# Optimization experiments

Measured on AMD Instinct MI355X. Metric: run time of the kernel, lower is better.

Reference implementation:

```python
import jax, jax.numpy as jnp
import numpy as np

B, S, D = 2, 2048, 2048
H, G, HD = 16, 8, 128          # query heads, kv groups, head_dim
GS = H // G                     # group size (queries per kv head)
EPS = 1e-6


def _rmsnorm(x, scale):
    # Qwen3-compatible: upcast to f32, rms over last dim, scale
    xf = x.astype(jnp.float32)
    ms = jnp.mean(xf * xf, axis=-1, keepdims=True)
    return (xf * jax.lax.rsqrt(ms + EPS) * scale).astype(x.dtype)


def _rope(x, cos, sin):
    # x: (b, h, s, hd); cos/sin: (s, hd) rotate-half convention
    hd = x.shape[-1]
    x1, x2 = x[..., : hd // 2], x[..., hd // 2 :]
    rotated = jnp.concatenate([-x2, x1], axis=-1)
    s = x.shape[2]
    c = cos[None, None, :s, :]
    sn = sin[None, None, :s, :]
    return (x * c + rotated * sn).astype(x.dtype)


def setup_inputs() -> dict:
    key = jax.random.key(0)
    ks = jax.random.split(key, 8)
    x = jax.random.normal(ks[0], (B, S, D), jnp.float32)
    # causal mask: True = masked (future positions)
    mask = jnp.triu(jnp.ones((S, S), dtype=bool), k=1)
    # RoPE tables, rotate-half convention (cat(angles, angles))
    inv_freq = 1.0 / (10000.0 ** (np.arange(0, HD, 2, dtype=np.float32) / HD))
    angles = np.arange(S, dtype=np.float32)[:, None] * inv_freq[None, :]
    angles = np.concatenate([angles, angles], axis=-1)  # (S, HD)
    cos = jnp.asarray(np.cos(angles))
    sin = jnp.asarray(np.sin(angles))
    std = 0.02
    Wq = jax.random.normal(ks[1], (D, H * HD), jnp.float32) * std
    Wk = jax.random.normal(ks[2], (D, G * HD), jnp.float32) * std
    Wv = jax.random.normal(ks[3], (D, G * HD), jnp.float32) * std
    Wo = jax.random.normal(ks[4], (H * HD, D), jnp.float32) * std
    q_scale = jnp.ones((HD,), jnp.float32)
    k_scale = jnp.ones((HD,), jnp.float32)
    return {"x": x, "mask": mask, "cos": cos, "sin": sin,
            "Wq": Wq, "Wk": Wk, "Wv": Wv, "Wo": Wo,
            "q_scale": q_scale, "k_scale": k_scale}


def reference(x, mask, cos, sin, Wq, Wk, Wv, Wo, q_scale, k_scale):
    b, s, _ = x.shape
    q = (x @ Wq).reshape(b, s, H, HD).transpose(0, 2, 1, 3)   # (b,H,s,hd)
    k = (x @ Wk).reshape(b, s, G, HD).transpose(0, 2, 1, 3)   # (b,G,s,hd)
    v = (x @ Wv).reshape(b, s, G, HD).transpose(0, 2, 1, 3)   # (b,G,s,hd)
    q = _rmsnorm(q, q_scale)
    k = _rmsnorm(k, k_scale)
    q = _rope(q, cos, sin)
    k = _rope(k, cos, sin)
    # grouped attention: avoid repeat_interleave by grouping query heads
    qg = q.reshape(b, G, GS, s, HD)
    scores = jnp.einsum('bghqd,bgkd->bghqk', qg, k)           # (b,G,GS,s,s)
    scores = jnp.where(mask[None, None, None, :, :], -jnp.inf, scores)
    weights = jax.nn.softmax(scores / jnp.sqrt(jnp.float32(HD)), axis=-1)
    ctx = jnp.einsum('bghqk,bgkd->bghqd', weights, v)          # (b,G,GS,s,hd)
    ctx = ctx.reshape(b, H, s, HD).transpose(0, 2, 1, 3).reshape(b, s, H * HD)
    return ctx @ Wo
```

## Files before the change

kernel.cpp:

```cpp
#include <hip/hip_runtime.h>
#include <stdint.h>

#define S_LEN 2048
#define NH 16
#define NG 8
#define HDIM 128

typedef __bf16 bf16x8 __attribute__((ext_vector_type(8)));
typedef float f32x4 __attribute__((ext_vector_type(4)));

#define MFMA16(a, b, c) __builtin_amdgcn_mfma_f32_16x16x32_bf16((a), (b), (c), 0, 0, 0)

__device__ __forceinline__ uint16_t f2bf(float f) {
  union { float f; uint32_t u; } v; v.f = f;
  return (uint16_t)((v.u + 0x7fffu + ((v.u >> 16) & 1u)) >> 16);
}

__device__ __forceinline__ void gload16(const void* g, void* l) {
  __builtin_amdgcn_global_load_lds(
      (__attribute__((address_space(1))) const void*)g,
      (__attribute__((address_space(3))) void*)l, 16, 0, 0);
}

__global__ __launch_bounds__(256) void cvt_x_kernel(
    const float* __restrict__ x, uint16_t* __restrict__ xb, int n4) {
  int i = blockIdx.x * 256 + threadIdx.x;
  if (i >= n4) return;
  float4 v = ((const float4*)x)[i];
  ushort4 o;
  o.x = f2bf(v.x); o.y = f2bf(v.y); o.z = f2bf(v.z); o.w = f2bf(v.w);
  ((ushort4*)xb)[i] = o;
}

__global__ __launch_bounds__(256) void trans_cvt_kernel(
    const float* __restrict__ src, uint16_t* __restrict__ dst, int K, int N) {
  __shared__ float T[32][33];
  int n0 = blockIdx.x * 32, k0 = blockIdx.y * 32;
  int tx = threadIdx.x & 31, ty = threadIdx.x >> 5;
  #pragma unroll
  for (int i = 0; i < 4; ++i)
    T[ty + i * 8][tx] = src[(size_t)(k0 + ty + i * 8) * N + n0 + tx];
  __syncthreads();
  #pragma unroll
  for (int i = 0; i < 4; ++i)
    dst[(size_t)(n0 + ty + i * 8) * K + k0 + tx] = f2bf(T[tx][ty + i * 8]);
}

__global__ __launch_bounds__(256) void gemm_bt_kernel(
    const uint16_t* __restrict__ A, const uint16_t* __restrict__ BT,
    float* __restrict__ C, int M, int N, int K) {
  __shared__ uint8_t smem[32768];
  uint16_t* As = (uint16_t*)smem;
  uint16_t* Bs = (uint16_t*)(smem + 16384);
  const int tid = threadIdx.x, lane = tid & 63, wid = tid >> 6;
  const int l15 = lane & 15, l4 = lane >> 4;
  const int m0 = blockIdx.y * 128, n0 = blockIdx.x * 128;
  const int wm = (wid >> 1) * 64, wn = (wid & 1) * 64;
  const int s_row = lane >> 3, s_col = (lane & 7) * 8;

  f32x4 acc[4][4];
  #pragma unroll
  for (int i = 0; i < 4; ++i)
    #pragma unroll
    for (int j = 0; j < 4; ++j) acc[i][j] = (f32x4){0.f, 0.f, 0.f, 0.f};

  for (int k0 = 0; k0 < K; k0 += 64) {
    #pragma unroll
    for (int i = 0; i < 4; ++i) {
      int chunk = wid * 4 + i;
      int row = chunk * 8 + s_row;
      gload16(A + (size_t)(m0 + row) * K + k0 + s_col, As + chunk * 512);
    }
    #pragma unroll
    for (int i = 0; i < 4; ++i) {
      int chunk = wid * 4 + i;
      int row = chunk * 8 + s_row;
      gload16(BT + (size_t)(n0 + row) * K + k0 + s_col, Bs + chunk * 512);
    }
    __syncthreads();
    #pragma unroll
    for (int kk = 0; kk < 2; ++kk) {
      bf16x8 af[4], bfr[4];
      #pragma unroll
      for (int mi = 0; mi < 4; ++mi)
        af[mi] = *(const bf16x8*)(As + (wm + mi * 16 + l15) * 64 + kk * 32 + l4 * 8);
      #pragma unroll
      for (int ni = 0; ni < 4; ++ni)
        bfr[ni] = *(const bf16x8*)(Bs + (wn + ni * 16 + l15) * 64 + kk * 32 + l4 * 8);
      #pragma unroll
      for (int mi = 0; mi < 4; ++mi)
        #pragma unroll
        for (int ni = 0; ni < 4; ++ni)
          acc[mi][ni] = MFMA16(af[mi], bfr[ni], acc[mi][ni]);
    }
    __syncthreads();
  }
  #pragma unroll
  for (int mi = 0; mi < 4; ++mi)
    #pragma unroll
    for (int ni = 0; ni < 4; ++ni) {
      float* dst = C + (size_t)(m0 + wm + mi * 16 + l4 * 4) * N + n0 + wn + ni * 16 + l15;
      #pragma unroll
      for (int r = 0; r < 4; ++r) dst[(size_t)r * N] = acc[mi][ni][r];
    }
}

__global__ __launch_bounds__(256) void qk_rope_kernel(
    const float* __restrict__ QKV, const float* __restrict__ cosb,
    const float* __restrict__ sinb, const float* __restrict__ qs,
    const float* __restrict__ ks, uint16_t* __restrict__ Qb,
    uint16_t* __restrict__ Kb) {
  const int task = blockIdx.x * 4 + (threadIdx.x >> 6);
  const int lane = threadIdx.x & 63;
  const int hh = task % 24;
  const int row = task / 24;
  const int s = row & (S_LEN - 1);
  const int b = row >> 11;
  const float c1 = cosb[s * 128 + lane], c2 = cosb[s * 128 + 64 + lane];
  const float s1 = sinb[s * 128 + lane], s2 = sinb[s * 128 + 64 + lane];
  const float* src = QKV + (size_t)row * 4096;
  float v1, v2, sc1, sc2, outscale;
  uint16_t* dst;
  if (hh < 16) {
    v1 = src[hh * 128 + lane]; v2 = src[hh * 128 + 64 + lane];
    sc1 = qs[lane]; sc2 = qs[lane + 64];
    outscale = 0.088388347648318447f;
    dst = Qb + ((size_t)(b * NH + hh) * S_LEN + s) * 128;
  } else {
    int g = hh - 16;
    v1 = src[2048 + g * 128 + lane]; v2 = src[2048 + g * 128 + 64 + lane];
    sc1 = ks[lane]; sc2 = ks[lane + 64];
    outscale = 1.0f;
    dst = Kb + ((size_t)(b * NG + g) * S_LEN + s) * 128;
  }
  float ss = v1 * v1 + v2 * v2;
  #pragma unroll
  for (int o = 1; o < 64; o <<= 1) ss += __shfl_xor(ss, o);
  float inv = rsqrtf(ss * (1.0f / 128.0f) + 1e-6f);
  float n1 = v1 * inv * sc1, n2 = v2 * inv * sc2;
  dst[lane] = f2bf((n1 * c1 - n2 * s1) * outscale);
  dst[lane + 64] = f2bf((n2 * c2 + n1 * s2) * outscale);
}

__global__ __launch_bounds__(256) void v_trans_kernel(
    const float* __restrict__ QKV, uint16_t* __restrict__ Vt) {
  __shared__ uint16_t T[128][72];
  const int s0 = blockIdx.x * 64;
  const int bg = blockIdx.y;
  const int b = bg >> 3, g = bg & 7;
  const int tid = threadIdx.x;
  const int tc = tid & 127, tr = tid >> 7;
  const float* src = QKV + ((size_t)(b * S_LEN + s0)) * 4096 + 3072 + g * 128;
  #pragma unroll
  for (int i = 0; i < 32; ++i) {
    int r = i * 2 + tr;
    T[tc][r] = f2bf(src[(size_t)r * 4096 + tc]);
  }
  __syncthreads();
  uint16_t* dst = Vt + (size_t)bg * 128 * S_LEN + s0;
  #pragma unroll
  for (int i = 0; i < 32; ++i) {
    int idx = i * 256 + tid;
    int d = idx >> 6, sof = idx & 63;
    dst[(size_t)d * S_LEN + sof] = T[d][sof];
  }
}

__global__ __launch_bounds__(256) void attn_kernel(
    const uint16_t* __restrict__ Qb, const uint16_t* __restrict__ Kb,
    const uint16_t* __restrict__ Vt, uint16_t* __restrict__ Ctx) {
  __shared__ uint8_t smem[65536 + 4 * 2304];
  const int tid = threadIdx.x, lane = tid & 63, wid = tid >> 6;
  uint16_t* Ps = (uint16_t*)(smem + 65536) + wid * 1152;
  const int l15 = lane & 15, l4 = lane >> 4;

  const int bh = blockIdx.y;
  const int b = bh >> 4, h = bh & 15;
  const int bg = b * NG + (h >> 1);

  const uint16_t* Qh = Qb + (size_t)bh * S_LEN * HDIM;
  const uint16_t* Kh = Kb + (size_t)bg * S_LEN * HDIM;
  const uint16_t* Vh = Vt + (size_t)bg * HDIM * S_LEN;

  const int k_row = lane >> 4, k_c = lane & 15;
  const int v_row = lane >> 3, v_c = lane & 7;

#define STAGE(kt_, buf_)                                                      \
  do {                                                                        \
    const int kv0_ = (kt_) * 64;                                              \
    uint16_t* KsB_ = (uint16_t*)(smem + (buf_) * 16384);                      \
    uint16_t* VsB_ = (uint16_t*)(smem + 32768 + (buf_) * 16384);              \
    _Pragma("unroll")                                                         \
    for (int i_ = 0; i_ < 4; ++i_) {                                          \
      int chunk_ = wid * 4 + i_;                                              \
      int row_ = chunk_ * 4 + k_row;                                          \
      int sc_ = (k_c ^ (row_ & 7)) * 8;                                       \
      gload16(Kh + (size_t)(kv0_ + row_) * HDIM + sc_, KsB_ + chunk_ * 512);  \
    }                                                                         \
    _Pragma("unroll")                                                         \
    for (int i_ = 0; i_ < 4; ++i_) {                                          \
      int chunk_ = wid * 4 + i_;                                              \
      int row_ = chunk_ * 8 + v_row;                                          \
      int sc_ = (v_c ^ (row_ & 7)) * 8;                                       \
      gload16(Vh + (size_t)row_ * S_LEN + kv0_ + sc_, VsB_ + chunk_ * 512);   \
    }                                                                         \
  } while (0)

  for (int half = 0; half < 2; ++half) {
    const int qtile = half ? (31 - (int)blockIdx.x) : (int)blockIdx.x;
    const int q0 = qtile * 64;
    const int qrow = q0 + wid * 16 + l15;

    bf16x8 qf[4];
    #pragma unroll
    for (int kk = 0; kk < 4; ++kk)
      qf[kk] = *(const bf16x8*)(Qh + (size_t)qrow * HDIM + kk * 32 + l4 * 8);

    f32x4 acc[8];
    #pragma unroll
    for (int i = 0; i < 8; ++i) acc[i] = (f32x4){0.f, 0.f, 0.f, 0.f};
    float mrun = -1e30f, lrun = 0.f;

    const int nt = qtile + 1;
    int cur = 0;
    STAGE(0, 0);
    asm volatile("s_waitcnt vmcnt(0)\ns_barrier" ::: "memory");

    for (int kt = 0; kt < nt; ++kt) {
      const int kv0 = kt * 64;
      if (kt + 1 < nt) STAGE(kt + 1, cur ^ 1);

      uint16_t* Ks = (uint16_t*)(smem + cur * 16384);
      uint16_t* Vs = (uint16_t*)(smem + 32768 + cur * 16384);

      f32x4 sc[4];
      #pragma unroll
      for (int i = 0; i < 4; ++i) sc[i] = (f32x4){0.f, 0.f, 0.f, 0.f};
      __builtin_amdgcn_s_setprio(1);
      #pragma unroll
      for (int kk = 0; kk < 4; ++kk) {
        #pragma unroll
        for (int kc = 0; kc < 4; ++kc) {
          int key = kc * 16 + l15;
          int cc = (kk * 4 + l4) ^ (key & 7);
          bf16x8 kf = *(const bf16x8*)(Ks + key * 128 + cc * 8);
          sc[kc] = MFMA16(kf, qf[kk], sc[kc]);
        }
      }
      __builtin_amdgcn_s_setprio(0);
      if (kt == nt - 1) {
        #pragma unroll
        for (int kc = 0; kc < 4; ++kc)
          #pragma unroll
          for (int r = 0; r < 4; ++r)
            if (kv0 + kc * 16 + l4 * 4 + r > qrow) sc[kc][r] = -1e30f;
      }
      float tmax = -1e30f;
      #pragma unroll
      for (int kc = 0; kc < 4; ++kc)
        #pragma unroll
        for (int r = 0; r < 4; ++r) tmax = fmaxf(tmax, sc[kc][r]);
      tmax = fmaxf(tmax, __shfl_xor(tmax, 16));
      tmax = fmaxf(tmax, __shfl_xor(tmax, 32));
      float mnew = fmaxf(mrun, tmax);
      float corr = __expf(mrun - mnew);
      float tsum = 0.f;
      #pragma unroll
      for (int kc = 0; kc < 4; ++kc) {
        float p0 = __expf(sc[kc][0] - mnew);
        float p1 = __expf(sc[kc][1] - mnew);
        float p2 = __expf(sc[kc][2] - mnew);
        float p3 = __expf(sc[kc][3] - mnew);
        tsum += (p0 + p1) + (p2 + p3);
        ushort4 pw;
        pw.x = f2bf(p0); pw.y = f2bf(p1); pw.z = f2bf(p2); pw.w = f2bf(p3);
        *(ushort4*)(Ps + l15 * 72 + kc * 16 + l4 * 4) = pw;
      }
      tsum += __shfl_xor(tsum, 16);
      tsum += __shfl_xor(tsum, 32);
      lrun = lrun * corr + tsum;
      mrun = mnew;
      #pragma unroll
      for (int d0 = 0; d0 < 8; ++d0) acc[d0] *= corr;

      __builtin_amdgcn_s_setprio(1);
      #pragma unroll
      for (int hf = 0; hf < 2; ++hf) {
        bf16x8 pf = *(const bf16x8*)(Ps + l15 * 72 + hf * 32 + l4 * 8);
        #pragma unroll
        for (int d0 = 0; d0 < 8; ++d0) {
          int d = d0 * 16 + l15;
          int cc = (hf * 4 + l4) ^ (d & 7);
          bf16x8 vf = *(const bf16x8*)(Vs + d * 64 + cc * 8);
          acc[d0] = MFMA16(vf, pf, acc[d0]);
        }
      }
      __builtin_amdgcn_s_setprio(0);

      asm volatile("s_waitcnt vmcnt(0)\ns_barrier" ::: "memory");
      cur ^= 1;
    }

    float inv = 1.0f / lrun;
    uint16_t* dst = Ctx + ((size_t)(b * S_LEN + qrow) * NH + h) * HDIM;
    #pragma unroll
    for (int d0 = 0; d0 < 8; ++d0) {
      ushort4 o;
      o.x = f2bf(acc[d0][0] * inv);
      o.y = f2bf(acc[d0][1] * inv);
      o.z = f2bf(acc[d0][2] * inv);
      o.w = f2bf(acc[d0][3] * inv);
      *(ushort4*)(dst + d0 * 16 + l4 * 4) = o;
    }
  }
#undef STAGE
}

extern "C" void kernel_launch(void* const* d_in, const int* in_sizes, int n_in,
                              void* d_out, int out_size, void* d_ws, size_t ws_size,
                              hipStream_t stream) {
  const float* x    = (const float*)d_in[0];
  const float* cosb = (const float*)d_in[2];
  const float* sinb = (const float*)d_in[3];
  const float* Wq   = (const float*)d_in[4];
  const float* Wk   = (const float*)d_in[5];
  const float* Wv   = (const float*)d_in[6];
  const float* Wo   = (const float*)d_in[7];
  const float* qs   = (const float*)d_in[8];
  const float* ks   = (const float*)d_in[9];

  char* ws = (char*)d_ws;
  uint16_t* Xb    = (uint16_t*)(ws);
  uint16_t* WallT = (uint16_t*)(ws + (16ull << 20));
  uint16_t* WoT   = (uint16_t*)(ws + (32ull << 20));
  float*    QKV   = (float*)   (ws + (40ull << 20));
  uint16_t* Qb    = (uint16_t*)(ws + (104ull << 20));
  uint16_t* Kb    = (uint16_t*)(ws + (120ull << 20));
  uint16_t* Vt    = (uint16_t*)(ws + (128ull << 20));
  uint16_t* Ctx   = (uint16_t*)(ws + (136ull << 20));
  float* out = (float*)d_out;

  cvt_x_kernel<<<8192, 256, 0, stream>>>(x, Xb, 2097152);
  trans_cvt_kernel<<<dim3(64, 64), 256, 0, stream>>>(Wq, WallT, 2048, 2048);
  trans_cvt_kernel<<<dim3(32, 64), 256, 0, stream>>>(Wk, WallT + 2048 * 2048, 2048, 1024);
  trans_cvt_kernel<<<dim3(32, 64), 256, 0, stream>>>(Wv, WallT + 3072 * 2048, 2048, 1024);
  trans_cvt_kernel<<<dim3(64, 64), 256, 0, stream>>>(Wo, WoT, 2048, 2048);
  gemm_bt_kernel<<<dim3(32, 32), 256, 0, stream>>>(Xb, WallT, QKV, 4096, 4096, 2048);
  qk_rope_kernel<<<24576, 256, 0, stream>>>(QKV, cosb, sinb, qs, ks, Qb, Kb);
  v_trans_kernel<<<dim3(32, 16), 256, 0, stream>>>(QKV, Vt);
  attn_kernel<<<dim3(16, 32), 256, 0, stream>>>(Qb, Kb, Vt, Ctx);
  gemm_bt_kernel<<<dim3(16, 32), 256, 0, stream>>>(Ctx, WoT, out, 4096, 2048, 2048);
}
```

Baseline: 392.3 us.

## Replace GEMM with 8-wave double-buffered pipelined kernel with swizzled LDS

Replaces the simple 128x128 single-buffered GEMM with a 512-thread kernel using 256x256 (QKV) or 128x256 (output) tiles. The K loop is split into 32-wide halves, double-buffered in dynamic LDS with XOR-swizzled layout, and global-to-LDS loads are interleaved with MFMA phases using barriers, waitcnt control and s_setprio. It also remaps block IDs for XCD-aware L2 locality. The aim is to hide load latency and avoid LDS bank conflicts, at the cost of large LDS use and a complex barrier schedule that lowers occupancy.

New measurement: 358.3 us. 8.7% less time.

```diff
diff --git a/kernel.cpp b/kernel.cpp
--- a/kernel.cpp
+++ b/kernel.cpp
@@ -46,63 +46,144 @@
     dst[(size_t)(n0 + ty + i * 8) * K + k0 + tx] = f2bf(T[tx][ty + i * 8]);
 }
 
-__global__ __launch_bounds__(256) void gemm_bt_kernel(
+template <int NISSUE>
+__device__ __forceinline__ void stage_half(const uint16_t* __restrict__ g,
+                                           int ldg, char* lds, int tid) {
+  #pragma unroll
+  for (int i = 0; i < NISSUE; ++i) {
+    int ch = i * 512 + tid;
+    int pair = ch >> 3, slotd = ch & 7;
+    int slotl = slotd ^ (pair & 7);
+    int row = pair * 2 + (slotl >> 2), c2 = slotl & 3;
+    gload16(g + (size_t)row * ldg + c2 * 8, lds + ch * 16);
+  }
+}
+
+__device__ __forceinline__ bf16x8 ldsfrag(const char* half_base, int row, int l4) {
+  int pair = row >> 1;
+  int slot = ((row & 1) << 2) | l4;
+  return *(const bf16x8*)(half_base + pair * 128 + ((slot ^ (pair & 7)) * 16));
+}
+
+#define BAR() asm volatile("s_barrier" ::: "memory")
+
+template <int BM>
+__global__ __launch_bounds__(512, 2) void gemm8p_kernel(
     const uint16_t* __restrict__ A, const uint16_t* __restrict__ BT,
-    float* __restrict__ C, int M, int N, int K) {
-  __shared__ uint8_t smem[32768];
-  uint16_t* As = (uint16_t*)smem;
-  uint16_t* Bs = (uint16_t*)(smem + 16384);
-  const int tid = threadIdx.x, lane = tid & 63, wid = tid >> 6;
+    float* __restrict__ C, int M, int N, int K, int gridN) {
+  extern __shared__ char smem[];
+  constexpr int MI = BM / 32;
+  constexpr int LA = BM / 128;
+  constexpr int ABYTES = BM * 64;
+  const int tid = threadIdx.x, lane = tid & 63;
+  const int wid = tid >> 6;
   const int l15 = lane & 15, l4 = lane >> 4;
-  const int m0 = blockIdx.y * 128, n0 = blockIdx.x * 128;
-  const int wm = (wid >> 1) * 64, wn = (wid & 1) * 64;
-  const int s_row = lane >> 3, s_col = (lane & 7) * 8;
-
-  f32x4 acc[4][4];
-  #pragma unroll
-  for (int i = 0; i < 4; ++i)
-    #pragma unroll
-    for (int j = 0; j < 4; ++j) acc[i][j] = (f32x4){0.f, 0.f, 0.f, 0.f};
-
-  for (int k0 = 0; k0 < K; k0 += 64) {
-    #pragma unroll
-    for (int i = 0; i < 4; ++i) {
-      int chunk = wid * 4 + i;
-      int row = chunk * 8 + s_row;
-      gload16(A + (size_t)(m0 + row) * K + k0 + s_col, As + chunk * 512);
-    }
-    #pragma unroll
-    for (int i = 0; i < 4; ++i) {
-      int chunk = wid * 4 + i;
-      int row = chunk * 8 + s_row;
-      gload16(BT + (size_t)(n0 + row) * K + k0 + s_col, Bs + chunk * 512);
-    }
-    __syncthreads();
-    #pragma unroll
-    for (int kk = 0; kk < 2; ++kk) {
-      bf16x8 af[4], bfr[4];
-      #pragma unroll
-      for (int mi = 0; mi < 4; ++mi)
-        af[mi] = *(const bf16x8*)(As + (wm + mi * 16 + l15) * 64 + kk * 32 + l4 * 8);
-      #pragma unroll
-      for (int ni = 0; ni < 4; ++ni)
-        bfr[ni] = *(const bf16x8*)(Bs + (wn + ni * 16 + l15) * 64 + kk * 32 + l4 * 8);
-      #pragma unroll
-      for (int mi = 0; mi < 4; ++mi)
-        #pragma unroll
-        for (int ni = 0; ni < 4; ++ni)
-          acc[mi][ni] = MFMA16(af[mi], bfr[ni], acc[mi][ni]);
-    }
-    __syncthreads();
-  }
-  #pragma unroll
-  for (int mi = 0; mi < 4; ++mi)
+  const int wm = wid >> 2, wn = wid & 3;
+
+  const int nwg = gridDim.x, bid = blockIdx.x;
+  const int cpx = nwg >> 3;
+  const int swz = (bid & 7) * cpx + (bid >> 3);
+  const int m0 = (swz / gridN) * BM, n0 = (swz % gridN) * 256;
+
+  const uint16_t* Ag = A + (size_t)m0 * K;
+  const uint16_t* Bg = BT + (size_t)n0 * K;
+  const int NT = K >> 6;
+
+#define ABASE(p, k) (smem + (((p) << 1) | (k)) * ABYTES)
+#define BBASE(p, k) (smem + 4 * ABYTES + (((p) << 1) | (k)) * 16384)
+
+  f32x4 acc[MI][4];
+  #pragma unroll
+  for (int mi = 0; mi < MI; ++mi)
+    #pragma unroll
+    for (int ni = 0; ni < 4; ++ni) acc[mi][ni] = (f32x4){0.f, 0.f, 0.f, 0.f};
+
+  stage_half<LA>(Ag, K, ABASE(0, 0), tid);
+  stage_half<2>(Bg, K, BBASE(0, 0), tid);
+  stage_half<LA>(Ag + 32, K, ABASE(0, 1), tid);
+  stage_half<2>(Bg + 32, K, BBASE(0, 1), tid);
+  stage_half<LA>(Ag + 64, K, ABASE(1, 0), tid);
+  stage_half<2>(Bg + 64, K, BBASE(1, 0), tid);
+  if constexpr (BM == 256) asm volatile("s_waitcnt vmcnt(4)" ::: "memory");
+  else                     asm volatile("s_waitcnt vmcnt(3)" ::: "memory");
+  BAR();
+
+  int par = 0;
+  const int arow = wm * (BM / 2) + l15;
+  for (int u = 0; u < NT; ++u, par ^= 1) {
+    const int k0 = u * 64;
+    bf16x8 af[MI], bf0, bf1;
+    #pragma unroll
+    for (int mi = 0; mi < MI; ++mi) af[mi] = ldsfrag(ABASE(par, 0), arow + mi * 16, l4);
+    bf0 = ldsfrag(BBASE(par, 0), wn * 64 + l15, l4);
+    bf1 = ldsfrag(BBASE(par, 0), wn * 64 + 16 + l15, l4);
+    if (u + 1 < NT) stage_half<LA>(Ag + (k0 + 96), K, ABASE(par ^ 1, 1), tid);
+    BAR();
+    __builtin_amdgcn_s_setprio(1);
+    #pragma unroll
+    for (int mi = 0; mi < MI; ++mi) {
+      acc[mi][0] = MFMA16(af[mi], bf0, acc[mi][0]);
+      acc[mi][1] = MFMA16(af[mi], bf1, acc[mi][1]);
+    }
+    __builtin_amdgcn_s_setprio(0);
+    BAR();
+    bf0 = ldsfrag(BBASE(par, 0), wn * 64 + 32 + l15, l4);
+    bf1 = ldsfrag(BBASE(par, 0), wn * 64 + 48 + l15, l4);
+    if (u + 1 < NT) stage_half<2>(Bg + (k0 + 96), K, BBASE(par ^ 1, 1), tid);
+    BAR();
+    __builtin_amdgcn_s_setprio(1);
+    #pragma unroll
+    for (int mi = 0; mi < MI; ++mi) {
+      acc[mi][2] = MFMA16(af[mi], bf0, acc[mi][2]);
+      acc[mi][3] = MFMA16(af[mi], bf1, acc[mi][3]);
+    }
+    __builtin_amdgcn_s_setprio(0);
+    BAR();
+    #pragma unroll
+    for (int mi = 0; mi < MI; ++mi) af[mi] = ldsfrag(ABASE(par, 1), arow + mi * 16, l4);
+    bf0 = ldsfrag(BBASE(par, 1), wn * 64 + 32 + l15, l4);
+    bf1 = ldsfrag(BBASE(par, 1), wn * 64 + 48 + l15, l4);
+    if (u + 2 < NT) stage_half<LA>(Ag + (k0 + 128), K, ABASE(par, 0), tid);
+    BAR();
+    __builtin_amdgcn_s_setprio(1);
+    #pragma unroll
+    for (int mi = 0; mi < MI; ++mi) {
+      acc[mi][2] = MFMA16(af[mi], bf0, acc[mi][2]);
+      acc[mi][3] = MFMA16(af[mi], bf1, acc[mi][3]);
+    }
+    __builtin_amdgcn_s_setprio(0);
+    BAR();
+    bf0 = ldsfrag(BBASE(par, 1), wn * 64 + l15, l4);
+    bf1 = ldsfrag(BBASE(par, 1), wn * 64 + 16 + l15, l4);
+    if (u + 2 < NT) stage_half<2>(Bg + (k0 + 128), K, BBASE(par, 0), tid);
+    BAR();
+    __builtin_amdgcn_s_setprio(1);
+    #pragma unroll
+    for (int mi = 0; mi < MI; ++mi) {
+      acc[mi][0] = MFMA16(af[mi], bf0, acc[mi][0]);
+      acc[mi][1] = MFMA16(af[mi], bf1, acc[mi][1]);
+    }
+    __builtin_amdgcn_s_setprio(0);
+    if (u + 2 < NT) {
+      if constexpr (BM == 256) asm volatile("s_waitcnt vmcnt(4)" ::: "memory");
+      else                     asm volatile("s_waitcnt vmcnt(3)" ::: "memory");
+    } else {
+      asm volatile("s_waitcnt vmcnt(0)" ::: "memory");
+    }
+    BAR();
+  }
+
+  #pragma unroll
+  for (int mi = 0; mi < MI; ++mi)
     #pragma unroll
     for (int ni = 0; ni < 4; ++ni) {
-      float* dst = C + (size_t)(m0 + wm + mi * 16 + l4 * 4) * N + n0 + wn + ni * 16 + l15;
+      float* dst = C + (size_t)(m0 + wm * (BM / 2) + mi * 16 + l4 * 4) * N +
+                   n0 + wn * 64 + ni * 16 + l15;
       #pragma unroll
       for (int r = 0; r < 4; ++r) dst[(size_t)r * N] = acc[mi][ni][r];
     }
+#undef ABASE
+#undef BBASE
 }
 
 __global__ __launch_bounds__(256) void qk_rope_kernel(
@@ -340,14 +421,19 @@
   uint16_t* Ctx   = (uint16_t*)(ws + (136ull << 20));
   float* out = (float*)d_out;
 
+  hipFuncSetAttribute(reinterpret_cast<const void*>(&gemm8p_kernel<256>),
+                      hipFuncAttributeMaxDynamicSharedMemorySize, 131072);
+  hipFuncSetAttribute(reinterpret_cast<const void*>(&gemm8p_kernel<128>),
+                      hipFuncAttributeMaxDynamicSharedMemorySize, 98304);
+
   cvt_x_kernel<<<8192, 256, 0, stream>>>(x, Xb, 2097152);
   trans_cvt_kernel<<<dim3(64, 64), 256, 0, stream>>>(Wq, WallT, 2048, 2048);
   trans_cvt_kernel<<<dim3(32, 64), 256, 0, stream>>>(Wk, WallT + 2048 * 2048, 2048, 1024);
   trans_cvt_kernel<<<dim3(32, 64), 256, 0, stream>>>(Wv, WallT + 3072 * 2048, 2048, 1024);
   trans_cvt_kernel<<<dim3(64, 64), 256, 0, stream>>>(Wo, WoT, 2048, 2048);
-  gemm_bt_kernel<<<dim3(32, 32), 256, 0, stream>>>(Xb, WallT, QKV, 4096, 4096, 2048);
+  gemm8p_kernel<256><<<256, 512, 131072, stream>>>(Xb, WallT, QKV, 4096, 4096, 2048, 16);
   qk_rope_kernel<<<24576, 256, 0, stream>>>(QKV, cosb, sinb, qs, ks, Qb, Kb);
   v_trans_kernel<<<dim3(32, 16), 256, 0, stream>>>(QKV, Vt);
   attn_kernel<<<dim3(16, 32), 256, 0, stream>>>(Qb, Kb, Vt, Ctx);
-  gemm_bt_kernel<<<dim3(16, 32), 256, 0, stream>>>(Ctx, WoT, out, 4096, 2048, 2048);
-}
+  gemm8p_kernel<128><<<256, 512, 98304, stream>>>(Ctx, WoT, out, 4096, 2048, 2048, 8);
+}
```
